# Optimization experiments

Measured on AMD Instinct MI355X. Metric: run time of the kernel, lower is better.

Reference implementation:

```python
import math
import jax, jax.numpy as jnp
import numpy as np

S, H, E = 8192, 4096, 64          # tokens, hidden, experts
CAPACITY_FACTOR = 1.0
MIN_CAPACITY = 4


def setup_inputs() -> dict:
    key = jax.random.key(0)
    k1, k2 = jax.random.split(key)
    return {
        "gate_input": jax.random.normal(k1, (S, H), dtype=jnp.float32),
        "gate_weight": jax.random.normal(k2, (E, H), dtype=jnp.float32) * 0.02,
    }


def reference(gate_input, gate_weight):
    # Router projection (always fp32, bias-free Linear)
    logits = gate_input.astype(jnp.float32) @ gate_weight.astype(jnp.float32).T  # [S, E]
    gates = jax.nn.softmax(logits, axis=1)
    s, e = gates.shape
    # _capacity with capacity_factor*2 for top-2; static given shapes
    capacity = max(int(math.ceil(s * (CAPACITY_FACTOR * 2.0) / e)), MIN_CAPACITY)

    # top-2 expert selection
    _, sel = jax.lax.top_k(gates, 2)                       # [S, 2]
    mask1 = jax.nn.one_hot(sel[:, 0], e, dtype=jnp.int32)  # [S, E]
    mask2 = jax.nn.one_hot(sel[:, 1], e, dtype=jnp.int32)

    # cumsum-based slot assignment within each expert
    loc1 = jnp.cumsum(mask1, axis=0) - 1
    loc2 = jnp.cumsum(mask2, axis=0) - 1 + jnp.sum(mask1, axis=0, keepdims=True)

    # aux load-balancing loss (aux_loss_coef = 0 -> no gate rescale)
    me = jnp.mean(gates, axis=0)
    ce = jnp.mean(mask1.astype(jnp.float32), axis=0)
    l_aux = jnp.mean(me * ce) * e * e

    # drop tokens over capacity
    mask1 = mask1 * (loc1 < capacity).astype(jnp.int32)
    mask2 = mask2 * (loc2 < capacity).astype(jnp.int32)
    idx_in_exp1 = jnp.sum(loc1 * mask1, axis=1)            # [S]
    idx_in_exp2 = jnp.sum(loc2 * mask2, axis=1)

    m1f = mask1.astype(jnp.float32)
    m2f = mask2.astype(jnp.float32)
    w1 = jnp.max(gates * m1f, axis=1)
    w2 = jnp.max(gates * m2f, axis=1)
    denom = jnp.maximum(w1 + w2, jnp.finfo(jnp.float32).eps)
    w1 = w1 / denom
    w2 = w2 / denom

    gates1 = w1[:, None] * m1f                             # [S, E]
    gates2 = w2[:, None] * m2f
    loc1_sc = jax.nn.one_hot(idx_in_exp1, capacity, dtype=jnp.float32)  # [S, C]
    loc2_sc = jax.nn.one_hot(idx_in_exp2, capacity, dtype=jnp.float32)
    combine_weights = (gates1[:, :, None] * loc1_sc[:, None, :]
                       + gates2[:, :, None] * loc2_sc[:, None, :])      # [S, E, C]
    dispatch_mask = combine_weights > 0
    return l_aux, combine_weights, dispatch_mask
```

## Files before the change

### kernel.cpp

```cpp
#include <hip/hip_runtime.h>
#include <cstdint>
#include <cstddef>

constexpr int S = 8192;
constexpr int H = 4096;
constexpr int E = 64;
constexpr int CAP = 256;
constexpr int KSPLIT = 4;
constexpr int KCHUNK = H / KSPLIT;
constexpr int BK = 32;
constexpr int BM = 64;
constexpr long long SEC = (long long)S * E * CAP;

__global__ __launch_bounds__(256)
void k_gemm(const float* __restrict__ A, const float* __restrict__ W,
            float* __restrict__ part) {
    __shared__ float As[BK][BM + 4];
    __shared__ float Bs[BK][E + 4];
    const int tid = threadIdx.x;
    const int m0 = blockIdx.x * BM;
    const int kbase = blockIdx.y * KCHUNK;
    const int lr = tid >> 3;
    const int lc = (tid & 7) << 2;
    const int ty = tid >> 4;
    const int tx = tid & 15;

    float acc[4][4];
#pragma unroll
    for (int i = 0; i < 4; ++i)
#pragma unroll
        for (int j = 0; j < 4; ++j) acc[i][j] = 0.f;

    for (int kc = 0; kc < KCHUNK; kc += BK) {
        const float* ap = A + (size_t)(m0 + lr) * H + (kbase + kc + lc);
        const float4 av0 = *(const float4*)ap;
        const float4 av1 = *(const float4*)(ap + (size_t)32 * H);
        const float* bp = W + (size_t)lr * H + (kbase + kc + lc);
        const float4 bv0 = *(const float4*)bp;
        const float4 bv1 = *(const float4*)(bp + (size_t)32 * H);
        __syncthreads();
        As[lc + 0][lr] = av0.x; As[lc + 1][lr] = av0.y;
        As[lc + 2][lr] = av0.z; As[lc + 3][lr] = av0.w;
        As[lc + 0][lr + 32] = av1.x; As[lc + 1][lr + 32] = av1.y;
        As[lc + 2][lr + 32] = av1.z; As[lc + 3][lr + 32] = av1.w;
        Bs[lc + 0][lr] = bv0.x; Bs[lc + 1][lr] = bv0.y;
        Bs[lc + 2][lr] = bv0.z; Bs[lc + 3][lr] = bv0.w;
        Bs[lc + 0][lr + 32] = bv1.x; Bs[lc + 1][lr + 32] = bv1.y;
        Bs[lc + 2][lr + 32] = bv1.z; Bs[lc + 3][lr + 32] = bv1.w;
        __syncthreads();
#pragma unroll
        for (int kk = 0; kk < BK; ++kk) {
            const float4 a = *(const float4*)&As[kk][ty * 4];
            const float4 b = *(const float4*)&Bs[kk][tx * 4];
            acc[0][0] = fmaf(a.x, b.x, acc[0][0]);
            acc[0][1] = fmaf(a.x, b.y, acc[0][1]);
            acc[0][2] = fmaf(a.x, b.z, acc[0][2]);
            acc[0][3] = fmaf(a.x, b.w, acc[0][3]);
            acc[1][0] = fmaf(a.y, b.x, acc[1][0]);
            acc[1][1] = fmaf(a.y, b.y, acc[1][1]);
            acc[1][2] = fmaf(a.y, b.z, acc[1][2]);
            acc[1][3] = fmaf(a.y, b.w, acc[1][3]);
            acc[2][0] = fmaf(a.z, b.x, acc[2][0]);
            acc[2][1] = fmaf(a.z, b.y, acc[2][1]);
            acc[2][2] = fmaf(a.z, b.z, acc[2][2]);
            acc[2][3] = fmaf(a.z, b.w, acc[2][3]);
            acc[3][0] = fmaf(a.w, b.x, acc[3][0]);
            acc[3][1] = fmaf(a.w, b.y, acc[3][1]);
            acc[3][2] = fmaf(a.w, b.z, acc[3][2]);
            acc[3][3] = fmaf(a.w, b.w, acc[3][3]);
        }
    }
    float* P = part + (size_t)blockIdx.y * S * E;
#pragma unroll
    for (int i = 0; i < 4; ++i) {
        float4 v = make_float4(acc[i][0], acc[i][1], acc[i][2], acc[i][3]);
        *(float4*)&P[(size_t)(m0 + ty * 4 + i) * E + tx * 4] = v;
    }
}

__global__ __launch_bounds__(256)
void k_router(const float* __restrict__ part, int* __restrict__ e1a,
              int* __restrict__ e2a, float* __restrict__ g1a,
              float* __restrict__ g2a, float* __restrict__ sumg,
              int* __restrict__ cnt1) {
    const int lane = threadIdx.x & 63;
    const int gw = blockIdx.x * 4 + (threadIdx.x >> 6);
    float lsum = 0.f;
    int lcnt = 0;
    for (int s = gw; s < S; s += 256) {
        const float* p = part + (size_t)s * E + lane;
        float l = p[0] + p[(size_t)S * E] + p[2 * (size_t)S * E]
                + p[3 * (size_t)S * E];
        float m = l;
#pragma unroll
        for (int o = 32; o; o >>= 1) m = fmaxf(m, __shfl_xor(m, o));
        const float ex = __expf(l - m);
        float Z = ex;
#pragma unroll
        for (int o = 32; o; o >>= 1) Z += __shfl_xor(Z, o);
        const float g = ex / Z;
        lsum += g;
        float v1 = g; int i1 = lane;
#pragma unroll
        for (int o = 32; o; o >>= 1) {
            const float ov = __shfl_xor(v1, o);
            const int oi = __shfl_xor(i1, o);
            if (ov > v1 || (ov == v1 && oi < i1)) { v1 = ov; i1 = oi; }
        }
        float v2 = (lane == i1) ? -1.f : g; int i2 = lane;
#pragma unroll
        for (int o = 32; o; o >>= 1) {
            const float ov = __shfl_xor(v2, o);
            const int oi = __shfl_xor(i2, o);
            if (ov > v2 || (ov == v2 && oi < i2)) { v2 = ov; i2 = oi; }
        }
        if (i1 == lane) lcnt++;
        if (lane == 0) {
            e1a[s] = i1; e2a[s] = i2; g1a[s] = v1; g2a[s] = v2;
        }
    }
    atomicAdd(&sumg[lane], lsum);
    atomicAdd(&cnt1[lane], lcnt);
}

__global__ __launch_bounds__(64)
void k_assign(const int* __restrict__ e1a, const int* __restrict__ e2a,
              int* __restrict__ slot1a, int* __restrict__ slot2a) {
    const int e = blockIdx.x;
    const int lane = threadIdx.x;
    const unsigned long long below = (1ull << lane) - 1ull;
    int cnt = 0;
    for (int c = 0; c < S; c += 64) {
        const int s = c + lane;
        const bool m = (e1a[s] == e);
        const unsigned long long bal = __ballot(m);
        if (m) {
            const int rank = cnt + __popcll(bal & below);
            slot1a[s] = (rank < CAP) ? rank : -1;
        }
        cnt += __popcll(bal);
    }
    const int total1 = cnt;
    int cnt2 = 0;
    for (int c = 0; c < S; c += 64) {
        const int s = c + lane;
        const bool m = (e2a[s] == e);
        const unsigned long long bal = __ballot(m);
        if (m) {
            const int rank = total1 + cnt2 + __popcll(bal & below);
            slot2a[s] = (rank < CAP) ? rank : -1;
        }
        cnt2 += __popcll(bal);
    }
}

__global__ __launch_bounds__(256)
void k_scatter(const int* __restrict__ e1a, const int* __restrict__ e2a,
               const float* __restrict__ g1a, const float* __restrict__ g2a,
               const int* __restrict__ slot1a, const int* __restrict__ slot2a,
               const float* __restrict__ sumg, const int* __restrict__ cnt1,
               float* __restrict__ out) {
    const int s = blockIdx.x * 256 + threadIdx.x;
    float* comb = out + 1;
    float* mask = out + 1 + (size_t)SEC;
    const int sl1 = slot1a[s], sl2 = slot2a[s];
    const float w1 = (sl1 >= 0) ? g1a[s] : 0.f;
    const float w2 = (sl2 >= 0) ? g2a[s] : 0.f;
    const float denom = fmaxf(w1 + w2, 1.1920928955078125e-07f);
    if (sl1 >= 0) {
        const size_t off = ((size_t)s * E + e1a[s]) * CAP + sl1;
        comb[off] = w1 / denom;
        mask[off] = 1.f;
    }
    if (sl2 >= 0) {
        const size_t off = ((size_t)s * E + e2a[s]) * CAP + sl2;
        comb[off] = w2 / denom;
        mask[off] = 1.f;
    }
    if (blockIdx.x == 0 && threadIdx.x < 64) {
        const int lane = threadIdx.x;
        float v = sumg[lane] * (float)cnt1[lane];
#pragma unroll
        for (int o = 32; o; o >>= 1) v += __shfl_xor(v, o);
        if (lane == 0) out[0] = v * (float)E / ((float)S * (float)S);
    }
}

extern "C" void kernel_launch(void* const* d_in, const int* in_sizes, int n_in,
                              void* d_out, int out_size, void* d_ws,
                              size_t ws_size, hipStream_t stream) {
    const float* A = (const float*)d_in[0];
    const float* W = (const float*)d_in[1];
    float* out = (float*)d_out;

    char* ws = (char*)d_ws;
    float* part = (float*)ws;
    size_t off = (size_t)KSPLIT * S * E * sizeof(float);
    int* e1a = (int*)(ws + off);      off += (size_t)S * 4;
    int* e2a = (int*)(ws + off);      off += (size_t)S * 4;
    float* g1a = (float*)(ws + off);  off += (size_t)S * 4;
    float* g2a = (float*)(ws + off);  off += (size_t)S * 4;
    int* slot1a = (int*)(ws + off);   off += (size_t)S * 4;
    int* slot2a = (int*)(ws + off);   off += (size_t)S * 4;
    float* sumg = (float*)(ws + off); off += (size_t)E * 4;
    int* cnt1 = (int*)(ws + off);     off += (size_t)E * 4;

    hipMemsetAsync(sumg, 0, 2 * (size_t)E * 4, stream);
    hipMemsetAsync(d_out, 0, sizeof(float) * (size_t)(1 + 2 * SEC), stream);

    k_gemm<<<dim3(S / BM, KSPLIT), 256, 0, stream>>>(A, W, part);
    k_router<<<64, 256, 0, stream>>>(part, e1a, e2a, g1a, g2a, sumg, cnt1);
    k_assign<<<E, 64, 0, stream>>>(e1a, e2a, slot1a, slot2a);
    k_scatter<<<S / 256, 256, 0, stream>>>(e1a, e2a, g1a, g2a, slot1a, slot2a,
                                           sumg, cnt1, out);
}
```

Before: 1.275 ms.

## Enlarge GEMM block tile to 256 rows with 8x8 register tiles

```diff
diff --git a/kernel.cpp b/kernel.cpp
--- a/kernel.cpp
+++ b/kernel.cpp
@@ -6,10 +6,10 @@
 constexpr int H = 4096;
 constexpr int E = 64;
 constexpr int CAP = 256;
-constexpr int KSPLIT = 4;
+constexpr int KSPLIT = 8;
 constexpr int KCHUNK = H / KSPLIT;
 constexpr int BK = 32;
-constexpr int BM = 64;
+constexpr int BM = 256;
 constexpr long long SEC = (long long)S * E * CAP;
 
 __global__ __launch_bounds__(256)
@@ -22,27 +22,32 @@
     const int kbase = blockIdx.y * KCHUNK;
     const int lr = tid >> 3;
     const int lc = (tid & 7) << 2;
-    const int ty = tid >> 4;
-    const int tx = tid & 15;
-
-    float acc[4][4];
-#pragma unroll
-    for (int i = 0; i < 4; ++i)
-#pragma unroll
-        for (int j = 0; j < 4; ++j) acc[i][j] = 0.f;
+    const int ty = tid >> 3;
+    const int tx = tid & 7;
+
+    float acc[8][8];
+#pragma unroll
+    for (int i = 0; i < 8; ++i)
+#pragma unroll
+        for (int j = 0; j < 8; ++j) acc[i][j] = 0.f;
 
     for (int kc = 0; kc < KCHUNK; kc += BK) {
         const float* ap = A + (size_t)(m0 + lr) * H + (kbase + kc + lc);
-        const float4 av0 = *(const float4*)ap;
-        const float4 av1 = *(const float4*)(ap + (size_t)32 * H);
+        float4 av[8];
+#pragma unroll
+        for (int j = 0; j < 8; ++j)
+            av[j] = *(const float4*)(ap + (size_t)(32 * j) * H);
         const float* bp = W + (size_t)lr * H + (kbase + kc + lc);
         const float4 bv0 = *(const float4*)bp;
         const float4 bv1 = *(const float4*)(bp + (size_t)32 * H);
         __syncthreads();
-        As[lc + 0][lr] = av0.x; As[lc + 1][lr] = av0.y;
-        As[lc + 2][lr] = av0.z; As[lc + 3][lr] = av0.w;
-        As[lc + 0][lr + 32] = av1.x; As[lc + 1][lr + 32] = av1.y;
-        As[lc + 2][lr + 32] = av1.z; As[lc + 3][lr + 32] = av1.w;
+#pragma unroll
+        for (int j = 0; j < 8; ++j) {
+            As[lc + 0][lr + 32 * j] = av[j].x;
+            As[lc + 1][lr + 32 * j] = av[j].y;
+            As[lc + 2][lr + 32 * j] = av[j].z;
+            As[lc + 3][lr + 32 * j] = av[j].w;
+        }
         Bs[lc + 0][lr] = bv0.x; Bs[lc + 1][lr] = bv0.y;
         Bs[lc + 2][lr] = bv0.z; Bs[lc + 3][lr] = bv0.w;
         Bs[lc + 0][lr + 32] = bv1.x; Bs[lc + 1][lr + 32] = bv1.y;
@@ -50,31 +55,27 @@
         __syncthreads();
 #pragma unroll
         for (int kk = 0; kk < BK; ++kk) {
-            const float4 a = *(const float4*)&As[kk][ty * 4];
-            const float4 b = *(const float4*)&Bs[kk][tx * 4];
-            acc[0][0] = fmaf(a.x, b.x, acc[0][0]);
-            acc[0][1] = fmaf(a.x, b.y, acc[0][1]);
-            acc[0][2] = fmaf(a.x, b.z, acc[0][2]);
-            acc[0][3] = fmaf(a.x, b.w, acc[0][3]);
-            acc[1][0] = fmaf(a.y, b.x, acc[1][0]);
-            acc[1][1] = fmaf(a.y, b.y, acc[1][1]);
-            acc[1][2] = fmaf(a.y, b.z, acc[1][2]);
-            acc[1][3] = fmaf(a.y, b.w, acc[1][3]);
-            acc[2][0] = fmaf(a.z, b.x, acc[2][0]);
-            acc[2][1] = fmaf(a.z, b.y, acc[2][1]);
-            acc[2][2] = fmaf(a.z, b.z, acc[2][2]);
-            acc[2][3] = fmaf(a.z, b.w, acc[2][3]);
-            acc[3][0] = fmaf(a.w, b.x, acc[3][0]);
-            acc[3][1] = fmaf(a.w, b.y, acc[3][1]);
-            acc[3][2] = fmaf(a.w, b.z, acc[3][2]);
-            acc[3][3] = fmaf(a.w, b.w, acc[3][3]);
+            const float4 a0 = *(const float4*)&As[kk][ty * 8];
+            const float4 a1 = *(const float4*)&As[kk][ty * 8 + 4];
+            const float4 b0 = *(const float4*)&Bs[kk][tx * 8];
+            const float4 b1 = *(const float4*)&Bs[kk][tx * 8 + 4];
+            const float a[8] = {a0.x, a0.y, a0.z, a0.w, a1.x, a1.y, a1.z, a1.w};
+            const float b[8] = {b0.x, b0.y, b0.z, b0.w, b1.x, b1.y, b1.z, b1.w};
+#pragma unroll
+            for (int i = 0; i < 8; ++i)
+#pragma unroll
+                for (int j = 0; j < 8; ++j)
+                    acc[i][j] = fmaf(a[i], b[j], acc[i][j]);
         }
     }
     float* P = part + (size_t)blockIdx.y * S * E;
 #pragma unroll
-    for (int i = 0; i < 4; ++i) {
-        float4 v = make_float4(acc[i][0], acc[i][1], acc[i][2], acc[i][3]);
-        *(float4*)&P[(size_t)(m0 + ty * 4 + i) * E + tx * 4] = v;
+    for (int i = 0; i < 8; ++i) {
+        const size_t row = (size_t)(m0 + ty * 8 + i);
+        float4 v0 = make_float4(acc[i][0], acc[i][1], acc[i][2], acc[i][3]);
+        float4 v1 = make_float4(acc[i][4], acc[i][5], acc[i][6], acc[i][7]);
+        *(float4*)&P[row * E + tx * 8] = v0;
+        *(float4*)&P[row * E + tx * 8 + 4] = v1;
     }
 }
 
@@ -89,8 +90,10 @@
     int lcnt = 0;
     for (int s = gw; s < S; s += 256) {
         const float* p = part + (size_t)s * E + lane;
-        float l = p[0] + p[(size_t)S * E] + p[2 * (size_t)S * E]
-                + p[3 * (size_t)S * E];
+        float l = 0.f;
+#pragma unroll
+        for (int j = 0; j < KSPLIT; ++j)
+            l += p[(size_t)j * S * E];
         float m = l;
 #pragma unroll
         for (int o = 32; o; o >>= 1) m = fmaxf(m, __shfl_xor(m, o));
```

Result: no change. 1.274 ms (-0.0%).
